# Optimization experiments

Measured on AMD Instinct MI355X. Metric: run time of the kernel, lower is better.

Reference implementation:

```python
import jax, jax.numpy as jnp
import numpy as np

GROUP_SIZE = 128

def setup_inputs() -> dict:
    key = jax.random.key(0)
    k1, k2, k3, k4 = jax.random.split(key, 4)
    in_f, out_f = 4096, 4096
    num_groups = (in_f + GROUP_SIZE - 1) // GROUP_SIZE  # 32
    x = jax.random.normal(k1, (4, 2048, in_f), dtype=jnp.float32)
    qweight = jax.random.randint(k2, (out_f, in_f), 0, 16, dtype=jnp.int32)
    scales = jax.random.uniform(k3, (out_f, num_groups), dtype=jnp.float32)
    bias = jax.random.normal(k4, (out_f,), dtype=jnp.float32)
    return {"x": x, "qweight": qweight, "scales": scales, "bias": bias}

def reference(x, qweight, scales, bias):
    out_f, in_f = qweight.shape
    # group-wise dequantize: broadcast each per-group scale over its columns
    scale_full = jnp.repeat(scales, GROUP_SIZE, axis=1)[:, :in_f]  # [out, in]
    weight = qweight.astype(scales.dtype) * scale_full             # [out, in]
    # F.linear(x, weight, bias) == x @ weight.T + bias
    return jnp.einsum('bsi,oi->bso', x, weight) + bias
```

## Files before the change

### kernel.cpp

```cpp
#include <hip/hip_runtime.h>
#include <hip/hip_bf16.h>

typedef __bf16 bf16_t;
typedef __bf16 bf16x8 __attribute__((ext_vector_type(8)));
typedef float  f32x4  __attribute__((ext_vector_type(4)));

static constexpr int M_ = 8192;
static constexpr int N_ = 4096;
static constexpr int K_ = 4096;

static constexpr int BM = 256, BN = 256, BK = 64;
static constexpr int NT = K_ / BK;
static constexpr int LDS_TILE = BM * BK;

__device__ __forceinline__ void load_lds16(const bf16_t* g, bf16_t* l) {
  __builtin_amdgcn_global_load_lds(
      (const __attribute__((address_space(1))) void*)g,
      (__attribute__((address_space(3))) void*)l,
      16, 0, 0);
}

__global__ __launch_bounds__(256) void cvt_x_kernel(const float* __restrict__ x,
                                                    bf16_t* __restrict__ xb) {
  const size_t i = ((size_t)blockIdx.x * 256 + threadIdx.x) * 8;
  const float4 f0 = *(const float4*)(x + i);
  const float4 f1 = *(const float4*)(x + i + 4);
  bf16x8 o;
  o[0] = (bf16_t)f0.x; o[1] = (bf16_t)f0.y; o[2] = (bf16_t)f0.z; o[3] = (bf16_t)f0.w;
  o[4] = (bf16_t)f1.x; o[5] = (bf16_t)f1.y; o[6] = (bf16_t)f1.z; o[7] = (bf16_t)f1.w;
  *(bf16x8*)(xb + i) = o;
}

__global__ __launch_bounds__(256) void dequant_kernel(const int* __restrict__ q,
                                                      const float* __restrict__ s,
                                                      bf16_t* __restrict__ wb) {
  const size_t base = ((size_t)blockIdx.x * 256 + threadIdx.x) * 8;
  const int o  = (int)(base >> 12);
  const int ii = (int)(base & 4095);
  const float sc = s[(o << 5) + (ii >> 7)];
  const int4 q0 = *(const int4*)(q + base);
  const int4 q1 = *(const int4*)(q + base + 4);
  bf16x8 w;
  w[0] = (bf16_t)((float)q0.x * sc); w[1] = (bf16_t)((float)q0.y * sc);
  w[2] = (bf16_t)((float)q0.z * sc); w[3] = (bf16_t)((float)q0.w * sc);
  w[4] = (bf16_t)((float)q1.x * sc); w[5] = (bf16_t)((float)q1.y * sc);
  w[6] = (bf16_t)((float)q1.z * sc); w[7] = (bf16_t)((float)q1.w * sc);
  *(bf16x8*)(wb + base) = w;
}

__global__ __launch_bounds__(512, 2) void gemm_kernel(const bf16_t* __restrict__ A,
                                                      const bf16_t* __restrict__ B,
                                                      const float* __restrict__ bias,
                                                      float* __restrict__ C) {
  __shared__ __align__(16) bf16_t As[2][LDS_TILE];
  __shared__ __align__(16) bf16_t Bs[2][LDS_TILE];

  const int tid  = threadIdx.x;
  const int lane = tid & 63;
  const int wave = tid >> 6;
  const int ln = lane & 15;
  const int lq = lane >> 4;
  const int wm = wave >> 2;
  const int wn = wave & 3;

  const int bid = blockIdx.x;
  const int wg  = (bid & 7) * 64 + (bid >> 3);
  const int bn  = (wg & 15) * BN;
  const int bm  = (wg >> 4) * BM;

  const int r_sub = tid >> 3;
  const int g_col = (((tid & 7) ^ (r_sub & 7)) * 8);
  const size_t a_off = (size_t)(bm + r_sub) * K_ + g_col;
  const size_t b_off = (size_t)(bn + r_sub) * K_ + g_col;
  const int lds_off = tid * 8;

  const int kx0 = (lq * 8) ^ ((ln & 7) * 8);
  const int kx1 = (32 + lq * 8) ^ ((ln & 7) * 8);
  const int a_rb = (wm * 128 + ln) * BK;
  const int b_rb = (wn * 64 + ln) * BK;

  f32x4 acc[8][4] = {};

#pragma unroll
  for (int c = 0; c < 4; ++c)
    load_lds16(A + a_off + (size_t)c * 64 * K_, &As[0][c * 4096 + lds_off]);
#pragma unroll
  for (int c = 0; c < 4; ++c)
    load_lds16(B + b_off + (size_t)c * 64 * K_, &Bs[0][c * 4096 + lds_off]);

  for (int t = 0; t < NT; ++t) {
    const int buf = t & 1;
    if (t + 1 < NT) {
      const size_t kt1 = (size_t)(t + 1) * BK;
#pragma unroll
      for (int c = 0; c < 4; ++c)
        load_lds16(A + a_off + kt1 + (size_t)c * 64 * K_, &As[buf ^ 1][c * 4096 + lds_off]);
#pragma unroll
      for (int c = 0; c < 4; ++c)
        load_lds16(B + b_off + kt1 + (size_t)c * 64 * K_, &Bs[buf ^ 1][c * 4096 + lds_off]);
      asm volatile("s_waitcnt vmcnt(8)" ::: "memory");
    } else {
      asm volatile("s_waitcnt vmcnt(0)" ::: "memory");
    }
    __builtin_amdgcn_s_barrier();
    __builtin_amdgcn_sched_barrier(0);

    const bf16_t* as = As[buf];
    const bf16_t* bs = Bs[buf];
    bf16x8 af[4][2], bq[4][2];

#pragma unroll
    for (int i = 0; i < 4; ++i) {
      af[i][0] = *(const bf16x8*)(as + a_rb + i * 16 * BK + kx0);
      af[i][1] = *(const bf16x8*)(as + a_rb + i * 16 * BK + kx1);
    }
#pragma unroll
    for (int j = 0; j < 2; ++j) {
      bq[j][0] = *(const bf16x8*)(bs + b_rb + j * 16 * BK + kx0);
      bq[j][1] = *(const bf16x8*)(bs + b_rb + j * 16 * BK + kx1);
    }
    __builtin_amdgcn_s_setprio(1);
#pragma unroll
    for (int i = 0; i < 4; ++i)
#pragma unroll
      for (int j = 0; j < 2; ++j) {
        acc[i][j] = __builtin_amdgcn_mfma_f32_16x16x32_bf16(af[i][0], bq[j][0], acc[i][j], 0, 0, 0);
        acc[i][j] = __builtin_amdgcn_mfma_f32_16x16x32_bf16(af[i][1], bq[j][1], acc[i][j], 0, 0, 0);
      }
    __builtin_amdgcn_s_setprio(0);

#pragma unroll
    for (int j = 2; j < 4; ++j) {
      bq[j][0] = *(const bf16x8*)(bs + b_rb + j * 16 * BK + kx0);
      bq[j][1] = *(const bf16x8*)(bs + b_rb + j * 16 * BK + kx1);
    }
    __builtin_amdgcn_s_setprio(1);
#pragma unroll
    for (int i = 0; i < 4; ++i)
#pragma unroll
      for (int j = 2; j < 4; ++j) {
        acc[i][j] = __builtin_amdgcn_mfma_f32_16x16x32_bf16(af[i][0], bq[j][0], acc[i][j], 0, 0, 0);
        acc[i][j] = __builtin_amdgcn_mfma_f32_16x16x32_bf16(af[i][1], bq[j][1], acc[i][j], 0, 0, 0);
      }
    __builtin_amdgcn_s_setprio(0);

#pragma unroll
    for (int i = 0; i < 4; ++i) {
      af[i][0] = *(const bf16x8*)(as + a_rb + (i + 4) * 16 * BK + kx0);
      af[i][1] = *(const bf16x8*)(as + a_rb + (i + 4) * 16 * BK + kx1);
    }
    __builtin_amdgcn_s_setprio(1);
#pragma unroll
    for (int i = 0; i < 4; ++i)
#pragma unroll
      for (int j = 2; j < 4; ++j) {
        acc[i + 4][j] = __builtin_amdgcn_mfma_f32_16x16x32_bf16(af[i][0], bq[j][0], acc[i + 4][j], 0, 0, 0);
        acc[i + 4][j] = __builtin_amdgcn_mfma_f32_16x16x32_bf16(af[i][1], bq[j][1], acc[i + 4][j], 0, 0, 0);
      }
    __builtin_amdgcn_s_setprio(0);

    __builtin_amdgcn_s_setprio(1);
#pragma unroll
    for (int i = 0; i < 4; ++i)
#pragma unroll
      for (int j = 0; j < 2; ++j) {
        acc[i + 4][j] = __builtin_amdgcn_mfma_f32_16x16x32_bf16(af[i][0], bq[j][0], acc[i + 4][j], 0, 0, 0);
        acc[i + 4][j] = __builtin_amdgcn_mfma_f32_16x16x32_bf16(af[i][1], bq[j][1], acc[i + 4][j], 0, 0, 0);
      }
    __builtin_amdgcn_s_setprio(0);

    __builtin_amdgcn_s_barrier();
  }

#pragma unroll
  for (int j = 0; j < 4; ++j) {
    const int col = bn + wn * 64 + j * 16 + ln;
    const float bv = bias[col];
#pragma unroll
    for (int i = 0; i < 8; ++i) {
      const int row0 = bm + wm * 128 + i * 16 + lq * 4;
      float* cp = C + (size_t)row0 * N_ + col;
#pragma unroll
      for (int r = 0; r < 4; ++r) {
        *cp = acc[i][j][r] + bv;
        cp += N_;
      }
    }
  }
}

extern "C" void kernel_launch(void* const* d_in, const int* in_sizes, int n_in,
                              void* d_out, int out_size, void* d_ws, size_t ws_size,
                              hipStream_t stream) {
  const float* x    = (const float*)d_in[0];
  const int*   qw   = (const int*)d_in[1];
  const float* sc   = (const float*)d_in[2];
  const float* bias = (const float*)d_in[3];
  float* out = (float*)d_out;

  bf16_t* xb = (bf16_t*)d_ws;
  bf16_t* wb = xb + (size_t)M_ * K_;

  cvt_x_kernel<<<(int)(((size_t)M_ * K_) / (256 * 8)), 256, 0, stream>>>(x, xb);
  dequant_kernel<<<(int)(((size_t)N_ * K_) / (256 * 8)), 256, 0, stream>>>(qw, sc, wb);

  const int nwg = (N_ / BN) * (M_ / BM);
  gemm_kernel<<<nwg, 512, 0, stream>>>(xb, wb, bias, out);
}
```

Before: 551.5 us.

## Split GEMM tiles into half-tiles with staggered prefetch pipeline

```diff
diff --git a/kernel.cpp b/kernel.cpp
--- a/kernel.cpp
+++ b/kernel.cpp
@@ -11,7 +11,8 @@
 
 static constexpr int BM = 256, BN = 256, BK = 64;
 static constexpr int NT = K_ / BK;
-static constexpr int LDS_TILE = BM * BK;
+static constexpr int HT_ELEMS  = 128 * 64;
+static constexpr int BUF_ELEMS = 2 * HT_ELEMS;
 
 __device__ __forceinline__ void load_lds16(const bf16_t* g, bf16_t* l) {
   __builtin_amdgcn_global_load_lds(
@@ -19,6 +20,8 @@
       (__attribute__((address_space(3))) void*)l,
       16, 0, 0);
 }
+
+#define MFMA16(a, b, c) __builtin_amdgcn_mfma_f32_16x16x32_bf16((a), (b), (c), 0, 0, 0)
 
 __global__ __launch_bounds__(256) void cvt_x_kernel(const float* __restrict__ x,
                                                     bf16_t* __restrict__ xb) {
@@ -52,8 +55,8 @@
                                                       const bf16_t* __restrict__ B,
                                                       const float* __restrict__ bias,
                                                       float* __restrict__ C) {
-  __shared__ __align__(16) bf16_t As[2][LDS_TILE];
-  __shared__ __align__(16) bf16_t Bs[2][LDS_TILE];
+  __shared__ __align__(16) bf16_t As[2 * BUF_ELEMS];
+  __shared__ __align__(16) bf16_t Bs[2 * BUF_ELEMS];
 
   const int tid  = threadIdx.x;
   const int lane = tid & 63;
@@ -69,116 +72,138 @@
   const int bm  = (wg >> 4) * BM;
 
   const int r_sub = tid >> 3;
-  const int g_col = (((tid & 7) ^ (r_sub & 7)) * 8);
-  const size_t a_off = (size_t)(bm + r_sub) * K_ + g_col;
-  const size_t b_off = (size_t)(bn + r_sub) * K_ + g_col;
+  const int g_col = ((tid & 7) ^ (r_sub & 7)) * 8;
+  const size_t a_base = (size_t)(bm + r_sub) * K_ + g_col;
+  const size_t b_base = (size_t)(bn + r_sub) * K_ + g_col;
   const int lds_off = tid * 8;
+
+  auto stageA = [&](int t, int h) {
+    bf16_t* d = As + (t & 1) * BUF_ELEMS + h * HT_ELEMS + lds_off;
+    const bf16_t* s = A + a_base + (size_t)(h * 128) * K_ + (size_t)t * BK;
+    load_lds16(s, d);
+    load_lds16(s + (size_t)64 * K_, d + 4096);
+  };
+  auto stageB = [&](int t, int h) {
+    bf16_t* d = Bs + (t & 1) * BUF_ELEMS + h * HT_ELEMS + lds_off;
+    const bf16_t* s = B + b_base + (size_t)(h * 128) * K_ + (size_t)t * BK;
+    load_lds16(s, d);
+    load_lds16(s + (size_t)64 * K_, d + 4096);
+  };
 
   const int kx0 = (lq * 8) ^ ((ln & 7) * 8);
   const int kx1 = (32 + lq * 8) ^ ((ln & 7) * 8);
-  const int a_rb = (wm * 128 + ln) * BK;
-  const int b_rb = (wn * 64 + ln) * BK;
+  const int a_row_off = (wm * 16 + ln) * 64;
+  const int b_row_off = (wn * 32 + ln) * 64;
 
   f32x4 acc[8][4] = {};
 
-#pragma unroll
-  for (int c = 0; c < 4; ++c)
-    load_lds16(A + a_off + (size_t)c * 64 * K_, &As[0][c * 4096 + lds_off]);
-#pragma unroll
-  for (int c = 0; c < 4; ++c)
-    load_lds16(B + b_off + (size_t)c * 64 * K_, &Bs[0][c * 4096 + lds_off]);
-
-  for (int t = 0; t < NT; ++t) {
-    const int buf = t & 1;
-    if (t + 1 < NT) {
-      const size_t kt1 = (size_t)(t + 1) * BK;
-#pragma unroll
-      for (int c = 0; c < 4; ++c)
-        load_lds16(A + a_off + kt1 + (size_t)c * 64 * K_, &As[buf ^ 1][c * 4096 + lds_off]);
-#pragma unroll
-      for (int c = 0; c < 4; ++c)
-        load_lds16(B + b_off + kt1 + (size_t)c * 64 * K_, &Bs[buf ^ 1][c * 4096 + lds_off]);
-      asm volatile("s_waitcnt vmcnt(8)" ::: "memory");
+  stageA(0, 0); stageB(0, 0); stageB(0, 1); stageA(0, 1);
+  stageA(1, 0); stageB(1, 0); stageB(1, 1);
+  asm volatile("s_waitcnt vmcnt(6)" ::: "memory");
+  __builtin_amdgcn_s_barrier();
+
+  for (int T = 0; T < NT; ++T) {
+    const bf16_t* as = As + (T & 1) * BUF_ELEMS;
+    const bf16_t* bs = Bs + (T & 1) * BUF_ELEMS;
+    bf16x8 af[4][2], bqA[2][2], bqB[2][2];
+
+#pragma unroll
+    for (int i = 0; i < 4; ++i) {
+      const bf16_t* p = as + a_row_off + i * 2048;
+      af[i][0] = *(const bf16x8*)(p + kx0);
+      af[i][1] = *(const bf16x8*)(p + kx1);
+    }
+#pragma unroll
+    for (int j = 0; j < 2; ++j) {
+      const bf16_t* p = bs + b_row_off + j * 1024;
+      bqA[j][0] = *(const bf16x8*)(p + kx0);
+      bqA[j][1] = *(const bf16x8*)(p + kx1);
+    }
+    if (T + 1 < NT) stageA(T + 1, 1);
+    asm volatile("s_waitcnt lgkmcnt(8)" ::: "memory");
+    __builtin_amdgcn_s_barrier();
+    asm volatile("s_waitcnt lgkmcnt(0)" ::: "memory");
+    __builtin_amdgcn_sched_barrier(0);
+    __builtin_amdgcn_s_setprio(1);
+#pragma unroll
+    for (int i = 0; i < 4; ++i)
+#pragma unroll
+      for (int j = 0; j < 2; ++j) {
+        acc[i][j] = MFMA16(af[i][0], bqA[j][0], acc[i][j]);
+        acc[i][j] = MFMA16(af[i][1], bqA[j][1], acc[i][j]);
+      }
+    __builtin_amdgcn_s_setprio(0);
+    __builtin_amdgcn_s_barrier();
+
+#pragma unroll
+    for (int j = 0; j < 2; ++j) {
+      const bf16_t* p = bs + HT_ELEMS + b_row_off + j * 1024;
+      bqB[j][0] = *(const bf16x8*)(p + kx0);
+      bqB[j][1] = *(const bf16x8*)(p + kx1);
+    }
+    if (T + 2 < NT) stageA(T + 2, 0);
+    __builtin_amdgcn_s_barrier();
+    asm volatile("s_waitcnt lgkmcnt(0)" ::: "memory");
+    __builtin_amdgcn_sched_barrier(0);
+    __builtin_amdgcn_s_setprio(1);
+#pragma unroll
+    for (int i = 0; i < 4; ++i)
+#pragma unroll
+      for (int j = 0; j < 2; ++j) {
+        acc[i][j + 2] = MFMA16(af[i][0], bqB[j][0], acc[i][j + 2]);
+        acc[i][j + 2] = MFMA16(af[i][1], bqB[j][1], acc[i][j + 2]);
+      }
+    __builtin_amdgcn_s_setprio(0);
+    __builtin_amdgcn_s_barrier();
+
+#pragma unroll
+    for (int i = 0; i < 4; ++i) {
+      const bf16_t* p = as + HT_ELEMS + a_row_off + i * 2048;
+      af[i][0] = *(const bf16x8*)(p + kx0);
+      af[i][1] = *(const bf16x8*)(p + kx1);
+    }
+    if (T + 2 < NT) stageB(T + 2, 0);
+    __builtin_amdgcn_s_barrier();
+    asm volatile("s_waitcnt lgkmcnt(0)" ::: "memory");
+    __builtin_amdgcn_sched_barrier(0);
+    __builtin_amdgcn_s_setprio(1);
+#pragma unroll
+    for (int i = 0; i < 4; ++i)
+#pragma unroll
+      for (int j = 0; j < 2; ++j) {
+        acc[i + 4][j + 2] = MFMA16(af[i][0], bqB[j][0], acc[i + 4][j + 2]);
+        acc[i + 4][j + 2] = MFMA16(af[i][1], bqB[j][1], acc[i + 4][j + 2]);
+      }
+    __builtin_amdgcn_s_setprio(0);
+    __builtin_amdgcn_s_barrier();
+
+    if (T + 2 < NT) {
+      stageB(T + 2, 1);
+      asm volatile("s_waitcnt vmcnt(6)" ::: "memory");
     } else {
       asm volatile("s_waitcnt vmcnt(0)" ::: "memory");
     }
     __builtin_amdgcn_s_barrier();
     __builtin_amdgcn_sched_barrier(0);
-
-    const bf16_t* as = As[buf];
-    const bf16_t* bs = Bs[buf];
-    bf16x8 af[4][2], bq[4][2];
-
-#pragma unroll
-    for (int i = 0; i < 4; ++i) {
-      af[i][0] = *(const bf16x8*)(as + a_rb + i * 16 * BK + kx0);
-      af[i][1] = *(const bf16x8*)(as + a_rb + i * 16 * BK + kx1);
-    }
-#pragma unroll
-    for (int j = 0; j < 2; ++j) {
-      bq[j][0] = *(const bf16x8*)(bs + b_rb + j * 16 * BK + kx0);
-      bq[j][1] = *(const bf16x8*)(bs + b_rb + j * 16 * BK + kx1);
-    }
-    __builtin_amdgcn_s_setprio(1);
-#pragma unroll
-    for (int i = 0; i < 4; ++i)
-#pragma unroll
-      for (int j = 0; j < 2; ++j) {
-        acc[i][j] = __builtin_amdgcn_mfma_f32_16x16x32_bf16(af[i][0], bq[j][0], acc[i][j], 0, 0, 0);
-        acc[i][j] = __builtin_amdgcn_mfma_f32_16x16x32_bf16(af[i][1], bq[j][1], acc[i][j], 0, 0, 0);
-      }
-    __builtin_amdgcn_s_setprio(0);
-
-#pragma unroll
-    for (int j = 2; j < 4; ++j) {
-      bq[j][0] = *(const bf16x8*)(bs + b_rb + j * 16 * BK + kx0);
-      bq[j][1] = *(const bf16x8*)(bs + b_rb + j * 16 * BK + kx1);
-    }
-    __builtin_amdgcn_s_setprio(1);
-#pragma unroll
-    for (int i = 0; i < 4; ++i)
-#pragma unroll
-      for (int j = 2; j < 4; ++j) {
-        acc[i][j] = __builtin_amdgcn_mfma_f32_16x16x32_bf16(af[i][0], bq[j][0], acc[i][j], 0, 0, 0);
-        acc[i][j] = __builtin_amdgcn_mfma_f32_16x16x32_bf16(af[i][1], bq[j][1], acc[i][j], 0, 0, 0);
-      }
-    __builtin_amdgcn_s_setprio(0);
-
-#pragma unroll
-    for (int i = 0; i < 4; ++i) {
-      af[i][0] = *(const bf16x8*)(as + a_rb + (i + 4) * 16 * BK + kx0);
-      af[i][1] = *(const bf16x8*)(as + a_rb + (i + 4) * 16 * BK + kx1);
-    }
-    __builtin_amdgcn_s_setprio(1);
-#pragma unroll
-    for (int i = 0; i < 4; ++i)
-#pragma unroll
-      for (int j = 2; j < 4; ++j) {
-        acc[i + 4][j] = __builtin_amdgcn_mfma_f32_16x16x32_bf16(af[i][0], bq[j][0], acc[i + 4][j], 0, 0, 0);
-        acc[i + 4][j] = __builtin_amdgcn_mfma_f32_16x16x32_bf16(af[i][1], bq[j][1], acc[i + 4][j], 0, 0, 0);
-      }
-    __builtin_amdgcn_s_setprio(0);
-
-    __builtin_amdgcn_s_setprio(1);
-#pragma unroll
-    for (int i = 0; i < 4; ++i)
-#pragma unroll
-      for (int j = 0; j < 2; ++j) {
-        acc[i + 4][j] = __builtin_amdgcn_mfma_f32_16x16x32_bf16(af[i][0], bq[j][0], acc[i + 4][j], 0, 0, 0);
-        acc[i + 4][j] = __builtin_amdgcn_mfma_f32_16x16x32_bf16(af[i][1], bq[j][1], acc[i + 4][j], 0, 0, 0);
-      }
-    __builtin_amdgcn_s_setprio(0);
-
+    __builtin_amdgcn_s_setprio(1);
+#pragma unroll
+    for (int i = 0; i < 4; ++i)
+#pragma unroll
+      for (int j = 0; j < 2; ++j) {
+        acc[i + 4][j] = MFMA16(af[i][0], bqA[j][0], acc[i + 4][j]);
+        acc[i + 4][j] = MFMA16(af[i][1], bqA[j][1], acc[i + 4][j]);
+      }
+    __builtin_amdgcn_s_setprio(0);
     __builtin_amdgcn_s_barrier();
   }
 
 #pragma unroll
   for (int j = 0; j < 4; ++j) {
-    const int col = bn + wn * 64 + j * 16 + ln;
+    const int col = bn + (j >> 1) * 128 + wn * 32 + (j & 1) * 16 + ln;
     const float bv = bias[col];
 #pragma unroll
     for (int i = 0; i < 8; ++i) {
-      const int row0 = bm + wm * 128 + i * 16 + lq * 4;
+      const int row0 = bm + (i >> 2) * 128 + (i & 3) * 32 + wm * 16 + lq * 4;
       float* cp = C + (size_t)row0 * N_ + col;
 #pragma unroll
       for (int r = 0; r < 4; ++r) {
```

New measurement: 491.3 us. -10.9%, faster.
